# Kernel tuning notes

Hardware: AMD Instinct MI355X
Metric: run time of the kernel (lower is better)

## Reference

```python
import jax, jax.numpy as jnp
import numpy as np

B = 16384      # batch of Monte Carlo paths
N = 100        # time steps
DIM_W = 3
DT = 0.01
SQRT_DT = DT ** 0.5
SIGMA0 = 0.5   # constant diffusion coefficient (concrete sigma = SIGMA0 * ones(B,1,DIM_W))


def _mlp(x, W1, b1, W2, b2, W3, b3):
    h = jax.nn.relu(x @ W1 + b1)
    h = jax.nn.relu(h @ W2 + b2)
    return h @ W3 + b3


def setup_inputs() -> dict:
    key = jax.random.key(0)
    ks = jax.random.split(key, 8)
    s = 0.1  # modest weight scale for numerical sanity
    return {
        'y0': jnp.ones((1,), jnp.float32),
        'Y0': jnp.zeros((1, 1), jnp.float32),
        'zW1': s * jax.random.normal(ks[0], (2, 64), jnp.float32),
        'zb1': jnp.zeros((64,), jnp.float32),
        'zW2': s * jax.random.normal(ks[1], (64, 64), jnp.float32),
        'zb2': jnp.zeros((64,), jnp.float32),
        'zW3': s * jax.random.normal(ks[2], (64, 3), jnp.float32),
        'zb3': jnp.zeros((3,), jnp.float32),
        'qW1': s * jax.random.normal(ks[3], (2, 64), jnp.float32),
        'qb1': jnp.zeros((64,), jnp.float32),
        'qW2': s * jax.random.normal(ks[4], (64, 64), jnp.float32),
        'qb2': jnp.zeros((64,), jnp.float32),
        'qW3': s * jax.random.normal(ks[5], (64, 1), jnp.float32),
        'qb3': jnp.zeros((1,), jnp.float32),
        'dW': jax.random.normal(ks[6], (N, B, DIM_W), jnp.float32),
        'dZ': jax.random.normal(ks[7], (N, B, DIM_W), jnp.float32),
    }


def reference(y0, Y0, zW1, zb1, zW2, zb2, zW3, zb3,
              qW1, qb1, qW2, qb2, qW3, qb3, dW, dZ):
    y = jnp.broadcast_to(y0.reshape(1, 1), (B, 1))          # (B,1) state
    Y = jnp.broadcast_to(Y0, (B, 1))                         # (B,1) value process
    t = jnp.zeros((B, 1), jnp.float32)

    def step(carry, noise):
        y, Y, t, loss_acc = carry
        dWi, dZi = noise
        inp = jnp.concatenate([t, y], axis=1)                # (B,2)
        z = _mlp(inp, zW1, zb1, zW2, zb2, zW3, zb3)          # (B,3)
        q = _mlp(inp, qW1, qb1, qW2, qb2, qW3, qb3)          # (B,1)
        f = 0.5 * q * q                                      # generator (B,1)
        dw = dWi * SQRT_DT
        dz = dZi * SQRT_DT
        # sigma = SIGMA0 * ones(B,1,DIM_W); bmm(sigma, dw) = SIGMA0 * sum_j dw_j
        diffusion = SIGMA0 * jnp.sum(dw, axis=1, keepdims=True)
        y_new = y + q * DT + diffusion                       # mu = q
        Y_next = Y - f * DT + jnp.sum(z * dw, axis=1, keepdims=True)
        residual = Y_next - (Y - f * DT + jnp.sum(z * dz, axis=1, keepdims=True))
        loss_acc = loss_acc + jnp.mean(residual * residual)
        return (y_new, Y_next, t + DT, loss_acc), None

    (y, Y, t, total_residual_loss), _ = jax.lax.scan(
        step, (y, Y, t, jnp.float32(0.0)), (dW, dZ))
    terminal = y * y                                         # terminal_cost(y)
    terminal_loss = jnp.mean((Y - terminal) ** 2)
    return terminal_loss + total_residual_loss
```

## Files before the change

### kernel.cpp

```cpp
#include <hip/hip_runtime.h>
#include <hip/hip_bf16.h>

#define BATCH   16384
#define NSTEPS  100
#define DT_     0.01f
#define SQRTDT  0.1f
#define SIGMA0_ 0.5f

typedef _Float16  f16x2  __attribute__((ext_vector_type(2)));
typedef _Float16  f16x4  __attribute__((ext_vector_type(4)));
typedef _Float16  f16x8  __attribute__((ext_vector_type(8)));
typedef __fp16    h16x2  __attribute__((ext_vector_type(2)));
typedef float     f32x4  __attribute__((ext_vector_type(4)));

__global__ void zero_out_kernel(float* out) { if (threadIdx.x == 0) out[0] = 0.0f; }

static __device__ __forceinline__ f16x4 pk4(const f32x4& d) {
    union { h16x2 h[2]; f16x4 v; } c;
    c.h[0] = __builtin_amdgcn_cvt_pkrtz(d[0], d[1]);
    c.h[1] = __builtin_amdgcn_cvt_pkrtz(d[2], d[3]);
    return c.v;
}

struct N3 { float a, b, c; };
union HU { unsigned short u; _Float16 h; };

__launch_bounds__(256, 2)
__global__ void deepbsde_kernel(
    const float* __restrict__ y0,  const float* __restrict__ Y0,
    const float* __restrict__ zW1, const float* __restrict__ zb1,
    const float* __restrict__ zW2, const float* __restrict__ zb2,
    const float* __restrict__ zW3, const float* __restrict__ zb3,
    const float* __restrict__ qW1, const float* __restrict__ qb1,
    const float* __restrict__ qW2, const float* __restrict__ qb2,
    const float* __restrict__ qW3, const float* __restrict__ qb3,
    const float* __restrict__ dW,  const float* __restrict__ dZ,
    float* __restrict__ out)
{
    __shared__ __align__(16) _Float16 tbl[NSTEPS * 128];
    __shared__ unsigned short yh_ring[2][NSTEPS + 1][16];
    __shared__ float ffin[2][16], yTfin[2][16];
    __shared__ int   flags[2];

    const int tid  = threadIdx.x;
    const int lane = tid & 63;
    const int w    = tid >> 6;
    const int g    = w >> 1;
    const int flip = (((int)blockIdx.x >> 3) ^ ((int)blockIdx.x >> 8)) & 1;
    const bool isQ = ((w & 1) ^ flip) != 0;
    const int ln15 = lane & 15, q4 = lane >> 4;
    const int gw   = (blockIdx.x << 1) + g;
    const int pbase = gw << 4;

    const float y0v = y0[0], Y0v = Y0[0];
    if (tid < 2) flags[tid] = 0;
    if (tid < 32) { HU hu; hu.h = (_Float16)y0v; yh_ring[tid >> 4][0][tid & 15] = hu.u; }

    {
        float tt = 0.0f;
        for (int i = 0; i < NSTEPS; ++i) {
            int r = (tid - (i << 6)) & 255;
            if (r < 64) {
                int q4e = r >> 4, mlp_ = (r >> 3) & 1, m = r & 7;
                const float* Wp = mlp_ ? qW1 : zW1;
                const float* bp = mlp_ ? qb1 : zb1;
                int i0 = 2*m, i1 = 2*m + 1;
                int k0 = 32*(i0 >> 3) + 8*q4e + (i0 & 7);
                int k1 = 32*(i1 >> 3) + 8*q4e + (i1 & 7);
                _Float16 th = (_Float16)tt;
                f16x2 A = {(_Float16)Wp[k0], (_Float16)Wp[k1]};
                f16x2 C = {(_Float16)bp[k0], (_Float16)bp[k1]};
                f16x2 tv = {th, th};
                f16x2 v = A*tv + C;
                int idx = (i*4 + q4e)*16 + mlp_*8 + m;
                *(f16x2*)&tbl[idx << 1] = v;
            }
            tt += DT_;
        }
    }

    const float* W1p = isQ ? qW1 : zW1;
    const float* W2p = isQ ? qW2 : zW2;
    const float* b2p = isQ ? qb2 : zb2;

    f16x2 B1[8];
#pragma unroll
    for (int m = 0; m < 8; ++m) {
        int i0 = 2*m, i1 = 2*m + 1;
        int k0 = 32*(i0 >> 3) + 8*q4 + (i0 & 7);
        int k1 = 32*(i1 >> 3) + 8*q4 + (i1 & 7);
        B1[m] = (f16x2){(_Float16)W1p[64 + k0], (_Float16)W1p[64 + k1]};
    }
    f16x8 Af[4][2];
#pragma unroll
    for (int tN = 0; tN < 4; ++tN)
#pragma unroll
        for (int f = 0; f < 2; ++f)
#pragma unroll
            for (int j = 0; j < 8; ++j) {
                int k = 32*f + 8*q4 + j, n = 16*tN + ln15;
                Af[tN][f][j] = (_Float16)W2p[k*64 + n];
            }
    f32x4 b2v[4];
#pragma unroll
    for (int tN = 0; tN < 4; ++tN)
#pragma unroll
        for (int r = 0; r < 4; ++r)
            b2v[tN][r] = b2p[16*tN + 4*q4 + r];

    const int c3 = ln15 & 3;
    f16x8 A3[2];
#pragma unroll
    for (int fl = 0; fl < 2; ++fl)
#pragma unroll
        for (int j = 0; j < 8; ++j) {
            int tN = 2*fl + (j >> 2);
            int n  = 16*tN + 4*q4 + (j & 3);
            float wv = isQ ? ((c3 == 3) ? qW3[n]                 : 0.0f)
                           : ((c3 < 3)  ? SQRTDT * zW3[n*3 + c3] : 0.0f);
            A3[fl][j] = (_Float16)wv;
        }
    const f32x4 C3b = isQ ? (f32x4){0.0f, 0.0f, 0.0f, qb3[0]}
                          : (f32x4){SQRTDT*zb3[0], SQRTDT*zb3[1], SQRTDT*zb3[2], 0.0f};

    const float CSIG = SIGMA0_ * SQRTDT;
    const float NHDT = -0.5f * DT_;
    const f16x2 zero2h = {(_Float16)0.0f, (_Float16)0.0f};
    const f16x4 zero4h = {(_Float16)0.0f, (_Float16)0.0f, (_Float16)0.0f, (_Float16)0.0f};

    auto loadW = [&](int i, N3& d) {
        int ic = (i < NSTEPS) ? i : NSTEPS - 1;
        const float* p = dW + ((size_t)ic * BATCH + pbase + ln15) * 3;
        d.a = p[0]; d.b = p[1]; d.c = p[2];
    };
    auto loadZ = [&](int i, N3& d) {
        int ic = (i < NSTEPS) ? i : NSTEPS - 1;
        const float* p = dZ + ((size_t)ic * BATCH + pbase + ln15) * 3;
        d.a = p[0]; d.b = p[1]; d.c = p[2];
    };

    __syncthreads();

    if (!isQ) {
        float Ysum = 0.0f, acc = 0.0f;
        f16x8 tc0, tc1, td0, td1;
        { const f16x8* tp = (const f16x8*)(tbl + q4*32); tc0 = tp[0]; tc1 = tp[1]; }
        unsigned short ya, yb, yc, yd, ea, eb, ec, ed;

        auto zstep = [&](int i, unsigned short yu, const N3& nw, const N3& nz,
                         f16x8& t0, f16x8& t1, f16x8& u0, f16x8& u1) {
            int ip = i + 1; ip = (ip > NSTEPS - 1) ? NSTEPS - 1 : ip;
            { const f16x8* tp = (const f16x8*)(tbl + (ip*4 + q4)*32); u0 = tp[0]; u1 = tp[1]; }

            HU hu; hu.u = yu;
            const f16x2 yv = {hu.h, hu.h};
            union U8 { f16x8 v; f16x2 h[4]; };
            U8 T0; T0.v = t0; U8 T1; T1.v = t1;
            union { f16x2 h[4]; f16x8 v; } b0, b1;
#pragma unroll
            for (int m = 0; m < 4; ++m) {
                b0.h[m] = __builtin_elementwise_max((f16x2)(B1[m]*yv   + T0.h[m]), zero2h);
                b1.h[m] = __builtin_elementwise_max((f16x2)(B1[m+4]*yv + T1.h[m]), zero2h);
            }
            union { f16x4 q[4]; f16x8 o[2]; } Bh;
#pragma unroll
            for (int tN = 0; tN < 4; ++tN) {
                f32x4 d = b2v[tN];
                d = __builtin_amdgcn_mfma_f32_16x16x32_f16(Af[tN][0], b0.v, d, 0, 0, 0);
                d = __builtin_amdgcn_mfma_f32_16x16x32_f16(Af[tN][1], b1.v, d, 0, 0, 0);
                Bh.q[tN] = __builtin_elementwise_max(pk4(d), zero4h);
            }
            f32x4 P = C3b;
            P = __builtin_amdgcn_mfma_f32_16x16x32_f16(A3[0], Bh.o[0], P, 0, 0, 0);
            P = __builtin_amdgcn_mfma_f32_16x16x32_f16(A3[1], Bh.o[1], P, 0, 0, 0);

            float zdw = fmaf(P[2], nw.c, fmaf(P[1], nw.b, P[0]*nw.a));
            float zdz = fmaf(P[2], nz.c, fmaf(P[1], nz.b, P[0]*nz.a));
            Ysum += zdw;
            float r = zdw - zdz;
            acc = fmaf(r, r, acc);
        };

        {
            volatile int* qf = &flags[g];
            while (*qf < 4) { }
            ya = *(volatile unsigned short*)&yh_ring[g][0][ln15];
            yb = *(volatile unsigned short*)&yh_ring[g][1][ln15];
            yc = *(volatile unsigned short*)&yh_ring[g][2][ln15];
            yd = *(volatile unsigned short*)&yh_ring[g][3][ln15];
        }
        N3 w0,w1,w2,w3,w4,w5,w6,w7, z0,z1,z2,z3,z4,z5,z6,z7;
        loadW(0,w0); loadZ(0,z0); loadW(1,w1); loadZ(1,z1);
        loadW(2,w2); loadZ(2,z2); loadW(3,w3); loadZ(3,z3);
        loadW(4,w4); loadZ(4,z4); loadW(5,w5); loadZ(5,z5);
        loadW(6,w6); loadZ(6,z6); loadW(7,w7); loadZ(7,z7);

#pragma unroll 1
        for (int b = 0; b < 25; ++b) {
            int i = 4*b;
            if (b < 24) {
                int need = i + 8; if (need > NSTEPS) need = NSTEPS;
                volatile int* qf = &flags[g];
                while (*qf < need) { }
                ea = *(volatile unsigned short*)&yh_ring[g][i + 4][ln15];
                eb = *(volatile unsigned short*)&yh_ring[g][i + 5][ln15];
                ec = *(volatile unsigned short*)&yh_ring[g][i + 6][ln15];
                ed = *(volatile unsigned short*)&yh_ring[g][i + 7][ln15];
            }
            if ((b & 1) == 0) {
                zstep(i,     ya, w0, z0, tc0, tc1, td0, td1); loadW(i + 8,  w0); loadZ(i + 8,  z0);
                zstep(i + 1, yb, w1, z1, td0, td1, tc0, tc1); loadW(i + 9,  w1); loadZ(i + 9,  z1);
                zstep(i + 2, yc, w2, z2, tc0, tc1, td0, td1); loadW(i + 10, w2); loadZ(i + 10, z2);
                zstep(i + 3, yd, w3, z3, td0, td1, tc0, tc1); loadW(i + 11, w3); loadZ(i + 11, z3);
            } else {
                zstep(i,     ya, w4, z4, tc0, tc1, td0, td1); loadW(i + 8,  w4); loadZ(i + 8,  z4);
                zstep(i + 1, yb, w5, z5, td0, td1, tc0, tc1); loadW(i + 9,  w5); loadZ(i + 9,  z5);
                zstep(i + 2, yc, w6, z6, tc0, tc1, td0, td1); loadW(i + 10, w6); loadZ(i + 10, z6);
                zstep(i + 3, yd, w7, z7, td0, td1, tc0, tc1); loadW(i + 11, w7); loadZ(i + 11, z7);
            }
            ya = ea; yb = eb; yc = ec; yd = ed;
        }

        { volatile int* qf = &flags[g]; while (*qf < NSTEPS + 1) { } }
        float Fq = *(volatile float*)&ffin[g][ln15];
        float yT = *(volatile float*)&yTfin[g][ln15];
        float Yvf = Y0v + Fq + Ysum;
        float dterm = Yvf - yT*yT;
        acc = fmaf(dterm, dterm, acc);

        float val = (q4 == 0) ? acc : 0.0f;
#pragma unroll
        for (int off = 1; off < 64; off <<= 1) val += __shfl_xor(val, off);
        if (lane == 0) atomicAdd(out, val * (1.0f / BATCH));
    } else {
        __builtin_amdgcn_s_setprio(1);
        float y = y0v, Facc = 0.0f;
        f16x8 c0, c1, d0, d1;
        { const f16x8* tp = (const f16x8*)(tbl + q4*32); c0 = tp[2]; c1 = tp[3]; }

        auto qstep = [&](int j, const N3& nw, f16x8& t0, f16x8& t1, f16x8& u0, f16x8& u1) {
            int jp = j + 1; jp = (jp > NSTEPS - 1) ? NSTEPS - 1 : jp;
            { const f16x8* tp = (const f16x8*)(tbl + (jp*4 + q4)*32); u0 = tp[2]; u1 = tp[3]; }

            _Float16 yh = (_Float16)y;
            const f16x2 yv = {yh, yh};
            union U8 { f16x8 v; f16x2 h[4]; };
            U8 T0; T0.v = t0; U8 T1; T1.v = t1;
            union { f16x2 h[4]; f16x8 v; } b0, b1;
#pragma unroll
            for (int m = 0; m < 4; ++m) {
                b0.h[m] = __builtin_elementwise_max((f16x2)(B1[m]*yv   + T0.h[m]), zero2h);
                b1.h[m] = __builtin_elementwise_max((f16x2)(B1[m+4]*yv + T1.h[m]), zero2h);
            }
            union { f16x4 q[4]; f16x8 o[2]; } Bh;
#pragma unroll
            for (int tN = 0; tN < 4; ++tN) {
                f32x4 d = b2v[tN];
                d = __builtin_amdgcn_mfma_f32_16x16x32_f16(Af[tN][0], b0.v, d, 0, 0, 0);
                d = __builtin_amdgcn_mfma_f32_16x16x32_f16(Af[tN][1], b1.v, d, 0, 0, 0);
                Bh.q[tN] = __builtin_elementwise_max(pk4(d), zero4h);
            }
            f32x4 Pv = C3b;
            Pv = __builtin_amdgcn_mfma_f32_16x16x32_f16(A3[0], Bh.o[0], Pv, 0, 0, 0);
            Pv = __builtin_amdgcn_mfma_f32_16x16x32_f16(A3[1], Bh.o[1], Pv, 0, 0, 0);

            float qv = Pv[3];
            float snw = (nw.a + nw.b) + nw.c;
            Facc = fmaf(NHDT*qv, qv, Facc);
            y = fmaf(CSIG, snw, fmaf(qv, DT_, y));
            if (q4 == 0) {
                HU hu; hu.h = (_Float16)y;
                *(volatile unsigned short*)&yh_ring[g][j + 1][ln15] = hu.u;
            }
        };

        N3 n0,n1,n2,n3,n4,n5,n6,n7;
        loadW(0,n0); loadW(1,n1); loadW(2,n2); loadW(3,n3);
        loadW(4,n4); loadW(5,n5); loadW(6,n6); loadW(7,n7);

#pragma unroll 1
        for (int k = 0; k < 12; ++k) {
            int j = 8*k;
            qstep(j,     n0, c0, c1, d0, d1);  loadW(j + 8,  n0);
            qstep(j + 1, n1, d0, d1, c0, c1);  loadW(j + 9,  n1);
            qstep(j + 2, n2, c0, c1, d0, d1);  loadW(j + 10, n2);
            qstep(j + 3, n3, d0, d1, c0, c1);  loadW(j + 11, n3);
            __builtin_amdgcn_s_waitcnt(0xC07F);
            if (lane == 0) *(volatile int*)&flags[g] = j + 4;
            qstep(j + 4, n4, c0, c1, d0, d1);  loadW(j + 12, n4);
            qstep(j + 5, n5, d0, d1, c0, c1);  loadW(j + 13, n5);
            qstep(j + 6, n6, c0, c1, d0, d1);  loadW(j + 14, n6);
            qstep(j + 7, n7, d0, d1, c0, c1);  loadW(j + 15, n7);
            __builtin_amdgcn_s_waitcnt(0xC07F);
            if (lane == 0) *(volatile int*)&flags[g] = j + 8;
        }
        qstep(96, n0, c0, c1, d0, d1);
        qstep(97, n1, d0, d1, c0, c1);
        qstep(98, n2, c0, c1, d0, d1);
        qstep(99, n3, d0, d1, c0, c1);
        __builtin_amdgcn_s_waitcnt(0xC07F);
        if (lane == 0) *(volatile int*)&flags[g] = NSTEPS;

        if (q4 == 0) {
            *(volatile float*)&ffin[g][ln15]  = Facc;
            *(volatile float*)&yTfin[g][ln15] = y;
        }
        __builtin_amdgcn_s_waitcnt(0xC07F);
        if (lane == 0) *(volatile int*)&flags[g] = NSTEPS + 1;
    }
}

extern "C" void kernel_launch(void* const* d_in, const int* in_sizes, int n_in,
                              void* d_out, int out_size, void* d_ws, size_t ws_size,
                              hipStream_t stream)
{
    zero_out_kernel<<<1, 64, 0, stream>>>((float*)d_out);
    deepbsde_kernel<<<512, 256, 0, stream>>>(
        (const float*)d_in[0],  (const float*)d_in[1],
        (const float*)d_in[2],  (const float*)d_in[3],
        (const float*)d_in[4],  (const float*)d_in[5],
        (const float*)d_in[6],  (const float*)d_in[7],
        (const float*)d_in[8],  (const float*)d_in[9],
        (const float*)d_in[10], (const float*)d_in[11],
        (const float*)d_in[12], (const float*)d_in[13],
        (const float*)d_in[14], (const float*)d_in[15],
        (float*)d_out);
}
```

Before: 161.3 us.

## Split z-MLP work across two waves per group using even/odd time-step packing

Blocks grow from 256 to 384 threads: waves 0-1 run the serial q-recurrence and waves 2-5 evaluate the z network, two z waves per path group. Each z wave packs 8 paths times 2 interleaved time steps (even and odd) into the 16 MFMA columns, so each wave does half the steps. Ysum is then combined across the halves with a shuffle. The aim is to take the z consumer off the critical path of the q producer. The cost is more waves per CU, more register and LDS pressure, and a padded table stride.

```diff
diff --git a/kernel.cpp b/kernel.cpp
--- a/kernel.cpp
+++ b/kernel.cpp
@@ -6,6 +6,7 @@
 #define DT_     0.01f
 #define SQRTDT  0.1f
 #define SIGMA0_ 0.5f
+#define TSTRIDE 144
 
 typedef _Float16  f16x2  __attribute__((ext_vector_type(2)));
 typedef _Float16  f16x4  __attribute__((ext_vector_type(4)));
@@ -25,7 +26,7 @@
 struct N3 { float a, b, c; };
 union HU { unsigned short u; _Float16 h; };
 
-__launch_bounds__(256, 2)
+__launch_bounds__(384, 3)
 __global__ void deepbsde_kernel(
     const float* __restrict__ y0,  const float* __restrict__ Y0,
     const float* __restrict__ zW1, const float* __restrict__ zb1,
@@ -37,7 +38,7 @@
     const float* __restrict__ dW,  const float* __restrict__ dZ,
     float* __restrict__ out)
 {
-    __shared__ __align__(16) _Float16 tbl[NSTEPS * 128];
+    __shared__ __align__(16) _Float16 tbl[NSTEPS * TSTRIDE];
     __shared__ unsigned short yh_ring[2][NSTEPS + 1][16];
     __shared__ float ffin[2][16], yTfin[2][16];
     __shared__ int   flags[2];
@@ -45,9 +46,9 @@
     const int tid  = threadIdx.x;
     const int lane = tid & 63;
     const int w    = tid >> 6;
-    const int g    = w >> 1;
-    const int flip = (((int)blockIdx.x >> 3) ^ ((int)blockIdx.x >> 8)) & 1;
-    const bool isQ = ((w & 1) ^ flip) != 0;
+    const bool isQ = (w < 2);
+    const int g    = isQ ? w : ((w - 2) >> 1);
+    const int half = (w - 2) & 1;
     const int ln15 = lane & 15, q4 = lane >> 4;
     const int gw   = (blockIdx.x << 1) + g;
     const int pbase = gw << 4;
@@ -59,8 +60,8 @@
     {
         float tt = 0.0f;
         for (int i = 0; i < NSTEPS; ++i) {
-            int r = (tid - (i << 6)) & 255;
-            if (r < 64) {
+            int r = tid - ((i % 6) << 6);
+            if (r >= 0 && r < 64) {
                 int q4e = r >> 4, mlp_ = (r >> 3) & 1, m = r & 7;
                 const float* Wp = mlp_ ? qW1 : zW1;
                 const float* bp = mlp_ ? qb1 : zb1;
@@ -72,8 +73,8 @@
                 f16x2 C = {(_Float16)bp[k0], (_Float16)bp[k1]};
                 f16x2 tv = {th, th};
                 f16x2 v = A*tv + C;
-                int idx = (i*4 + q4e)*16 + mlp_*8 + m;
-                *(f16x2*)&tbl[idx << 1] = v;
+                int hw = i*TSTRIDE + q4e*32 + mlp_*16 + 2*m;
+                *(f16x2*)&tbl[hw] = v;
             }
             tt += DT_;
         }
@@ -128,29 +129,32 @@
     const f16x2 zero2h = {(_Float16)0.0f, (_Float16)0.0f};
     const f16x4 zero4h = {(_Float16)0.0f, (_Float16)0.0f, (_Float16)0.0f, (_Float16)0.0f};
 
-    auto loadW = [&](int i, N3& d) {
-        int ic = (i < NSTEPS) ? i : NSTEPS - 1;
-        const float* p = dW + ((size_t)ic * BATCH + pbase + ln15) * 3;
-        d.a = p[0]; d.b = p[1]; d.c = p[2];
-    };
-    auto loadZ = [&](int i, N3& d) {
-        int ic = (i < NSTEPS) ? i : NSTEPS - 1;
-        const float* p = dZ + ((size_t)ic * BATCH + pbase + ln15) * 3;
-        d.a = p[0]; d.b = p[1]; d.c = p[2];
-    };
-
     __syncthreads();
 
     if (!isQ) {
+        const int sodd = ln15 >> 3;
+        const int prow = 8*half + (ln15 & 7);
         float Ysum = 0.0f, acc = 0.0f;
+
+        auto loadNW = [&](int k, N3& d) {
+            int s = 2*k + sodd; if (s > NSTEPS - 1) s = NSTEPS - 1;
+            const float* p = dW + ((size_t)s * BATCH + pbase + prow) * 3;
+            d.a = p[0]; d.b = p[1]; d.c = p[2];
+        };
+        auto loadNZ = [&](int k, N3& d) {
+            int s = 2*k + sodd; if (s > NSTEPS - 1) s = NSTEPS - 1;
+            const float* p = dZ + ((size_t)s * BATCH + pbase + prow) * 3;
+            d.a = p[0]; d.b = p[1]; d.c = p[2];
+        };
+
         f16x8 tc0, tc1, td0, td1;
-        { const f16x8* tp = (const f16x8*)(tbl + q4*32); tc0 = tp[0]; tc1 = tp[1]; }
-        unsigned short ya, yb, yc, yd, ea, eb, ec, ed;
-
-        auto zstep = [&](int i, unsigned short yu, const N3& nw, const N3& nz,
+        { const f16x8* tp = (const f16x8*)(tbl + sodd*TSTRIDE + q4*32); tc0 = tp[0]; tc1 = tp[1]; }
+
+        auto zpass = [&](int k, unsigned short yu, const N3& nw, const N3& nz,
                          f16x8& t0, f16x8& t1, f16x8& u0, f16x8& u1) {
-            int ip = i + 1; ip = (ip > NSTEPS - 1) ? NSTEPS - 1 : ip;
-            { const f16x8* tp = (const f16x8*)(tbl + (ip*4 + q4)*32); u0 = tp[0]; u1 = tp[1]; }
+            int kp = k + 1; if (kp > 49) kp = 49;
+            { const f16x8* tp = (const f16x8*)(tbl + (2*kp + sodd)*TSTRIDE + q4*32);
+              u0 = tp[0]; u1 = tp[1]; }
 
             HU hu; hu.u = yu;
             const f16x2 yv = {hu.h, hu.h};
@@ -181,53 +185,49 @@
             acc = fmaf(r, r, acc);
         };
 
+        unsigned short yu0, yu1, eu0, eu1;
         {
             volatile int* qf = &flags[g];
             while (*qf < 4) { }
-            ya = *(volatile unsigned short*)&yh_ring[g][0][ln15];
-            yb = *(volatile unsigned short*)&yh_ring[g][1][ln15];
-            yc = *(volatile unsigned short*)&yh_ring[g][2][ln15];
-            yd = *(volatile unsigned short*)&yh_ring[g][3][ln15];
-        }
-        N3 w0,w1,w2,w3,w4,w5,w6,w7, z0,z1,z2,z3,z4,z5,z6,z7;
-        loadW(0,w0); loadZ(0,z0); loadW(1,w1); loadZ(1,z1);
-        loadW(2,w2); loadZ(2,z2); loadW(3,w3); loadZ(3,z3);
-        loadW(4,w4); loadZ(4,z4); loadW(5,w5); loadZ(5,z5);
-        loadW(6,w6); loadZ(6,z6); loadW(7,w7); loadZ(7,z7);
+            yu0 = *(volatile unsigned short*)&yh_ring[g][0 + sodd][prow];
+            yu1 = *(volatile unsigned short*)&yh_ring[g][2 + sodd][prow];
+        }
+        N3 s0w, s0z, s1w, s1z, s2w, s2z, s3w, s3z;
+        loadNW(0, s0w); loadNZ(0, s0z); loadNW(1, s1w); loadNZ(1, s1z);
+        loadNW(2, s2w); loadNZ(2, s2z); loadNW(3, s3w); loadNZ(3, s3z);
 
 #pragma unroll 1
         for (int b = 0; b < 25; ++b) {
-            int i = 4*b;
+            int k0_ = 2*b;
             if (b < 24) {
-                int need = i + 8; if (need > NSTEPS) need = NSTEPS;
                 volatile int* qf = &flags[g];
-                while (*qf < need) { }
-                ea = *(volatile unsigned short*)&yh_ring[g][i + 4][ln15];
-                eb = *(volatile unsigned short*)&yh_ring[g][i + 5][ln15];
-                ec = *(volatile unsigned short*)&yh_ring[g][i + 6][ln15];
-                ed = *(volatile unsigned short*)&yh_ring[g][i + 7][ln15];
+                while (*qf < 4*b + 8) { }
+                eu0 = *(volatile unsigned short*)&yh_ring[g][4*b + 4 + sodd][prow];
+                eu1 = *(volatile unsigned short*)&yh_ring[g][4*b + 6 + sodd][prow];
             }
             if ((b & 1) == 0) {
-                zstep(i,     ya, w0, z0, tc0, tc1, td0, td1); loadW(i + 8,  w0); loadZ(i + 8,  z0);
-                zstep(i + 1, yb, w1, z1, td0, td1, tc0, tc1); loadW(i + 9,  w1); loadZ(i + 9,  z1);
-                zstep(i + 2, yc, w2, z2, tc0, tc1, td0, td1); loadW(i + 10, w2); loadZ(i + 10, z2);
-                zstep(i + 3, yd, w3, z3, td0, td1, tc0, tc1); loadW(i + 11, w3); loadZ(i + 11, z3);
+                zpass(k0_,     yu0, s0w, s0z, tc0, tc1, td0, td1);
+                loadNW(k0_ + 4, s0w); loadNZ(k0_ + 4, s0z);
+                zpass(k0_ + 1, yu1, s1w, s1z, td0, td1, tc0, tc1);
+                loadNW(k0_ + 5, s1w); loadNZ(k0_ + 5, s1z);
             } else {
-                zstep(i,     ya, w4, z4, tc0, tc1, td0, td1); loadW(i + 8,  w4); loadZ(i + 8,  z4);
-                zstep(i + 1, yb, w5, z5, td0, td1, tc0, tc1); loadW(i + 9,  w5); loadZ(i + 9,  z5);
-                zstep(i + 2, yc, w6, z6, tc0, tc1, td0, td1); loadW(i + 10, w6); loadZ(i + 10, z6);
-                zstep(i + 3, yd, w7, z7, td0, td1, tc0, tc1); loadW(i + 11, w7); loadZ(i + 11, z7);
-            }
-            ya = ea; yb = eb; yc = ec; yd = ed;
+                zpass(k0_,     yu0, s2w, s2z, tc0, tc1, td0, td1);
+                loadNW(k0_ + 4, s2w); loadNZ(k0_ + 4, s2z);
+                zpass(k0_ + 1, yu1, s3w, s3z, td0, td1, tc0, tc1);
+                loadNW(k0_ + 5, s3w); loadNZ(k0_ + 5, s3z);
+            }
+            yu0 = eu0; yu1 = eu1;
         }
 
         { volatile int* qf = &flags[g]; while (*qf < NSTEPS + 1) { } }
-        float Fq = *(volatile float*)&ffin[g][ln15];
-        float yT = *(volatile float*)&yTfin[g][ln15];
-        float Yvf = Y0v + Fq + Ysum;
-        float dterm = Yvf - yT*yT;
-        acc = fmaf(dterm, dterm, acc);
-
+        float Ys2 = Ysum + __shfl_xor(Ysum, 8);
+        if (sodd == 0) {
+            float Fq = *(volatile float*)&ffin[g][prow];
+            float yT = *(volatile float*)&yTfin[g][prow];
+            float Yvf = Y0v + Fq + Ys2;
+            float dterm = Yvf - yT*yT;
+            acc = fmaf(dterm, dterm, acc);
+        }
         float val = (q4 == 0) ? acc : 0.0f;
 #pragma unroll
         for (int off = 1; off < 64; off <<= 1) val += __shfl_xor(val, off);
@@ -238,9 +238,15 @@
         f16x8 c0, c1, d0, d1;
         { const f16x8* tp = (const f16x8*)(tbl + q4*32); c0 = tp[2]; c1 = tp[3]; }
 
+        auto loadW16 = [&](int i, N3& d) {
+            int ic = (i < NSTEPS) ? i : NSTEPS - 1;
+            const float* p = dW + ((size_t)ic * BATCH + pbase + ln15) * 3;
+            d.a = p[0]; d.b = p[1]; d.c = p[2];
+        };
+
         auto qstep = [&](int j, const N3& nw, f16x8& t0, f16x8& t1, f16x8& u0, f16x8& u1) {
             int jp = j + 1; jp = (jp > NSTEPS - 1) ? NSTEPS - 1 : jp;
-            { const f16x8* tp = (const f16x8*)(tbl + (jp*4 + q4)*32); u0 = tp[2]; u1 = tp[3]; }
+            { const f16x8* tp = (const f16x8*)(tbl + jp*TSTRIDE + q4*32); u0 = tp[2]; u1 = tp[3]; }
 
             _Float16 yh = (_Float16)y;
             const f16x2 yv = {yh, yh};
@@ -275,22 +281,22 @@
         };
 
         N3 n0,n1,n2,n3,n4,n5,n6,n7;
-        loadW(0,n0); loadW(1,n1); loadW(2,n2); loadW(3,n3);
-        loadW(4,n4); loadW(5,n5); loadW(6,n6); loadW(7,n7);
+        loadW16(0,n0); loadW16(1,n1); loadW16(2,n2); loadW16(3,n3);
+        loadW16(4,n4); loadW16(5,n5); loadW16(6,n6); loadW16(7,n7);
 
 #pragma unroll 1
         for (int k = 0; k < 12; ++k) {
             int j = 8*k;
-            qstep(j,     n0, c0, c1, d0, d1);  loadW(j + 8,  n0);
-            qstep(j + 1, n1, d0, d1, c0, c1);  loadW(j + 9,  n1);
-            qstep(j + 2, n2, c0, c1, d0, d1);  loadW(j + 10, n2);
-            qstep(j + 3, n3, d0, d1, c0, c1);  loadW(j + 11, n3);
+            qstep(j,     n0, c0, c1, d0, d1);  loadW16(j + 8,  n0);
+            qstep(j + 1, n1, d0, d1, c0, c1);  loadW16(j + 9,  n1);
+            qstep(j + 2, n2, c0, c1, d0, d1);  loadW16(j + 10, n2);
+            qstep(j + 3, n3, d0, d1, c0, c1);  loadW16(j + 11, n3);
             __builtin_amdgcn_s_waitcnt(0xC07F);
             if (lane == 0) *(volatile int*)&flags[g] = j + 4;
-            qstep(j + 4, n4, c0, c1, d0, d1);  loadW(j + 12, n4);
-            qstep(j + 5, n5, d0, d1, c0, c1);  loadW(j + 13, n5);
-            qstep(j + 6, n6, c0, c1, d0, d1);  loadW(j + 14, n6);
-            qstep(j + 7, n7, d0, d1, c0, c1);  loadW(j + 15, n7);
+            qstep(j + 4, n4, c0, c1, d0, d1);  loadW16(j + 12, n4);
+            qstep(j + 5, n5, d0, d1, c0, c1);  loadW16(j + 13, n5);
+            qstep(j + 6, n6, c0, c1, d0, d1);  loadW16(j + 14, n6);
+            qstep(j + 7, n7, d0, d1, c0, c1);  loadW16(j + 15, n7);
             __builtin_amdgcn_s_waitcnt(0xC07F);
             if (lane == 0) *(volatile int*)&flags[g] = j + 8;
         }
@@ -315,7 +321,7 @@
                               hipStream_t stream)
 {
     zero_out_kernel<<<1, 64, 0, stream>>>((float*)d_out);
-    deepbsde_kernel<<<512, 256, 0, stream>>>(
+    deepbsde_kernel<<<512, 384, 0, stream>>>(
         (const float*)d_in[0],  (const float*)d_in[1],
         (const float*)d_in[2],  (const float*)d_in[3],
         (const float*)d_in[4],  (const float*)d_in[5],
```

Result: slower. 207.2 us (+28.5%).
